# Performance work log

Measured on AMD Instinct MI355X. Metric: run time of the kernel, lower is better.

## Reference

```python
import jax, jax.numpy as jnp
import numpy as np

SCALE_CLS = 7.0
EPS = 1e-12

def _l2norm(x):
    # torch F.normalize: x / max(||x||_2, eps) along last dim
    n = jnp.sqrt(jnp.sum(x * x, axis=-1, keepdims=True))
    return x / jnp.maximum(n, EPS)

def setup_inputs() -> dict:
    key = jax.random.key(0)
    k1, k2 = jax.random.split(key)
    B, Q, C, D, H, W = 4, 75, 5, 512, 6, 6
    ftrain = jax.random.normal(k1, (B, Q, C, D, H, W), dtype=jnp.float32)
    ftest = jax.random.normal(k2, (B, Q, C, D, H, W), dtype=jnp.float32)
    return {"ftrain": ftrain, "ftest": ftest, "K": 28}

def reference(ftrain, ftest, K):
    B, Q, C, D, H, W = ftrain.shape
    P = H * W  # 36 spatial positions
    # spatial means -> [B,Q,C,1,D]
    ftest_mean = ftest.mean(axis=(4, 5))[:, :, :, None, :]
    ftrain_mean = ftrain.mean(axis=(4, 5))[:, :, :, None, :]
    # flatten spatial, move channel last -> [B,Q,C,P,D]
    ft = jnp.swapaxes(ftest.reshape(B, Q, C, D, P), 3, 4)
    fr = jnp.swapaxes(ftrain.reshape(B, Q, C, D, P), 3, 4)
    ft = _l2norm(ft)
    fr = _l2norm(fr)
    ftest_mean = _l2norm(ftest_mean)
    ftrain_mean = _l2norm(ftrain_mean)
    # global scores [B,Q,C]
    scores = SCALE_CLS * jnp.sum(jnp.squeeze(ftest_mean * ftrain_mean), axis=-1)
    # per-position scores [B,Q,C,P]
    ftrain_scores = SCALE_CLS * jnp.sum(ftest_mean * fr, axis=-1)
    ftest_scores = SCALE_CLS * jnp.sum(ft * ftrain_mean, axis=-1)
    # top-K positions (indices distinct, so one-hot-sum mask == gather)
    _, train_ind = jax.lax.top_k(ftrain_scores, K)  # [B,Q,C,K]
    _, test_ind = jax.lax.top_k(ftest_scores, K)
    # gather top-K spatial features and average -> [B,Q,C,D]
    ftest_fuse = jnp.take_along_axis(ft, test_ind[..., None], axis=3).sum(axis=3) / K
    ftrain_fuse = jnp.take_along_axis(fr, train_ind[..., None], axis=3).sum(axis=3) / K
    ftest_fuse = _l2norm(ftest_fuse)
    ftrain_fuse = _l2norm(ftrain_fuse)
    scores_final = SCALE_CLS * jnp.sum(ftest_fuse * ftrain_fuse, axis=-1)
    return (scores, scores_final)
```

## Files before the change

kernel.cpp:

```cpp
#include <hip/hip_runtime.h>
#include <stdint.h>

#define NGRP 1500
#define DD 512
#define PP 36
#define DP (DD*PP)
#define SWEEPS 19
#define SCALE_CLS 7.0f
#define EPS 1e-12f

__device__ __forceinline__ float waveRed(float x){
  #pragma unroll
  for (int off = 32; off; off >>= 1) x += __shfl_xor(x, off, 64);
  return x;
}

__global__ __launch_bounds__(256, 2)
void topk_fuse(const float* __restrict__ gtrain,
               const float* __restrict__ gtest,
               const int* __restrict__ Kp,
               float* __restrict__ out)
{
  __shared__ float s_rt[DD*9];
  __shared__ float s_rr[DD*9];
  __shared__ float s_tm[DD], s_rm[DD];
  __shared__ float s_q[PP], s_e[PP];
  __shared__ float s_a[PP], s_b[PP];
  __shared__ float s_st[PP], s_sr[PP];
  __shared__ float s_nt[PP], s_nr[PP];
  __shared__ float s_wt[PP], s_wr[PP];
  __shared__ float s_red[12];

  const int t    = threadIdx.x;
  const int lane = t & 63;
  const int wave = t >> 6;
  const int g    = blockIdx.x;
  const int K    = Kp[0];
  const int c    = t % 9;
  const int r    = t / 9;
  const bool act = t < 252;

  const float4* gt4 = (const float4*)(gtest  + (size_t)g * DP);
  const float4* gr4 = (const float4*)(gtrain + (size_t)g * DP);

  if (t < PP) { s_q[t] = 0.f; s_e[t] = 0.f; s_a[t] = 0.f; s_b[t] = 0.f; }

  float4 keepT[SWEEPS], keepR[SWEEPS];
  float4 q4 = {0,0,0,0}, e4 = {0,0,0,0};
  #pragma unroll
  for (int k = 0; k < SWEEPS; ++k) {
    const bool cact = (k < SWEEPS-1) ? act : (t < 72);
    float4 T = {0,0,0,0}, R = {0,0,0,0};
    if (cact) { int i = t + 252*k; T = gt4[i]; R = gr4[i]; }
    keepT[k] = T; keepR[k] = R;
    q4.x += T.x*T.x; q4.y += T.y*T.y; q4.z += T.z*T.z; q4.w += T.w*T.w;
    e4.x += R.x*R.x; e4.y += R.y*R.y; e4.z += R.z*R.z; e4.w += R.w*R.w;
    if (cact) {
      s_rt[t + 252*k] = T.x + T.y + T.z + T.w;
      s_rr[t + 252*k] = R.x + R.y + R.z + R.w;
    }
  }
  __syncthreads();

  float pm2 = 0.f, pr2 = 0.f, pmr = 0.f;
  #pragma unroll
  for (int h = 0; h < 2; ++h) {
    int d = t + 256*h;
    float st = 0.f, sr = 0.f;
    #pragma unroll
    for (int j = 0; j < 9; ++j) { st += s_rt[d*9 + j]; sr += s_rr[d*9 + j]; }
    float tm = st * (1.0f/36.0f), rm = sr * (1.0f/36.0f);
    s_tm[d] = tm; s_rm[d] = rm;
    pm2 += tm*tm; pr2 += rm*rm; pmr += tm*rm;
  }
  pm2 = waveRed(pm2); pr2 = waveRed(pr2); pmr = waveRed(pmr);
  if (lane == 0) { s_red[wave] = pm2; s_red[4+wave] = pr2; s_red[8+wave] = pmr; }
  __syncthreads();
  if (t == 0) {
    float m2 = s_red[0]+s_red[1]+s_red[2]+s_red[3];
    float r2 = s_red[4]+s_red[5]+s_red[6]+s_red[7];
    float mr = s_red[8]+s_red[9]+s_red[10]+s_red[11];
    float n1 = fmaxf(sqrtf(m2), EPS), n2 = fmaxf(sqrtf(r2), EPS);
    out[g] = SCALE_CLS * mr / (n1 * n2);
  }

  float4 a4 = {0,0,0,0}, b4 = {0,0,0,0};
  #pragma unroll
  for (int k = 0; k < SWEEPS; ++k) {
    int d = r + 28*k; if (d > 511) d = 511;
    float tm = s_tm[d], rm = s_rm[d];
    float4 T = keepT[k], R = keepR[k];
    a4.x += T.x*rm; a4.y += T.y*rm; a4.z += T.z*rm; a4.w += T.w*rm;
    b4.x += R.x*tm; b4.y += R.y*tm; b4.z += R.z*tm; b4.w += R.w*tm;
  }
  if (act) {
    int p0 = c*4;
    atomicAdd(&s_q[p0+0], q4.x); atomicAdd(&s_q[p0+1], q4.y);
    atomicAdd(&s_q[p0+2], q4.z); atomicAdd(&s_q[p0+3], q4.w);
    atomicAdd(&s_e[p0+0], e4.x); atomicAdd(&s_e[p0+1], e4.y);
    atomicAdd(&s_e[p0+2], e4.z); atomicAdd(&s_e[p0+3], e4.w);
    atomicAdd(&s_a[p0+0], a4.x); atomicAdd(&s_a[p0+1], a4.y);
    atomicAdd(&s_a[p0+2], a4.z); atomicAdd(&s_a[p0+3], a4.w);
    atomicAdd(&s_b[p0+0], b4.x); atomicAdd(&s_b[p0+1], b4.y);
    atomicAdd(&s_b[p0+2], b4.z); atomicAdd(&s_b[p0+3], b4.w);
  }
  __syncthreads();

  if (wave < 2 && lane < PP) {
    float q  = wave ? s_e[lane] : s_q[lane];
    float dm = wave ? s_b[lane] : s_a[lane];
    float n  = fmaxf(sqrtf(q), EPS);
    if (wave) { s_nr[lane] = n; s_sr[lane] = dm / n; }
    else      { s_nt[lane] = n; s_st[lane] = dm / n; }
  }
  __syncthreads();

  if (wave < 2 && lane < PP) {
    const float* sc = wave ? s_sr : s_st;
    const float* nn = wave ? s_nr : s_nt;
    float*       w  = wave ? s_wr : s_wt;
    float mine = sc[lane];
    int rank = 0;
    #pragma unroll
    for (int p = 0; p < PP; ++p) {
      float o = sc[p];
      rank += ((o > mine) || (o == mine && p < lane)) ? 1 : 0;
    }
    w[lane] = (rank < K) ? (1.0f / nn[lane]) : 0.f;
  }
  __syncthreads();

  float wt0=0,wt1=0,wt2=0,wt3=0, wr0=0,wr1=0,wr2=0,wr3=0;
  if (act) {
    wt0 = s_wt[4*c+0]; wt1 = s_wt[4*c+1]; wt2 = s_wt[4*c+2]; wt3 = s_wt[4*c+3];
    wr0 = s_wr[4*c+0]; wr1 = s_wr[4*c+1]; wr2 = s_wr[4*c+2]; wr3 = s_wr[4*c+3];
  }
  #pragma unroll
  for (int k = 0; k < SWEEPS; ++k) {
    const bool cact = (k < SWEEPS-1) ? act : (t < 72);
    if (cact) {
      float4 T = keepT[k], R = keepR[k];
      s_rt[t + 252*k] = T.x*wt0 + T.y*wt1 + T.z*wt2 + T.w*wt3;
      s_rr[t + 252*k] = R.x*wr0 + R.y*wr1 + R.z*wr2 + R.w*wr3;
    }
  }
  __syncthreads();
  float U2 = 0.f, V2 = 0.f, UV = 0.f;
  #pragma unroll
  for (int h = 0; h < 2; ++h) {
    int d = t + 256*h;
    float u = 0.f, v = 0.f;
    #pragma unroll
    for (int j = 0; j < 9; ++j) { u += s_rt[d*9 + j]; v += s_rr[d*9 + j]; }
    U2 += u*u; V2 += v*v; UV += u*v;
  }
  U2 = waveRed(U2); V2 = waveRed(V2); UV = waveRed(UV);
  if (lane == 0) { s_red[wave] = U2; s_red[4+wave] = V2; s_red[8+wave] = UV; }
  __syncthreads();
  if (t == 0) {
    float u2 = s_red[0]+s_red[1]+s_red[2]+s_red[3];
    float v2 = s_red[4]+s_red[5]+s_red[6]+s_red[7];
    float uv = s_red[8]+s_red[9]+s_red[10]+s_red[11];
    float nu = fmaxf(sqrtf(u2), EPS), nv = fmaxf(sqrtf(v2), EPS);
    out[NGRP + g] = SCALE_CLS * uv / (nu * nv);
  }
}

extern "C" void kernel_launch(void* const* d_in, const int* in_sizes, int n_in,
                              void* d_out, int out_size, void* d_ws, size_t ws_size,
                              hipStream_t stream)
{
  const float* ftrain = (const float*)d_in[0];
  const float* ftest  = (const float*)d_in[1];
  const int*   Kp     = (const int*)d_in[2];
  float*       out    = (float*)d_out;
  topk_fuse<<<NGRP, 256, 0, stream>>>(ftrain, ftest, Kp, out);
}
```

Baseline: 268.9 us.

## Stage full tiles in LDS via direct global-to-LDS loads with 512 threads

Replaces the register-held float4 sweeps with asynchronous global_load_lds transfers that copy each group's full test and train tiles (144 KB of LDS) into shared memory. The block grows to 512 threads with one channel per thread. Partial waitcnt overlaps the test-tile reductions with the train-tile load. Per-position reductions now run as strided LDS loops, and the top-K fuse becomes a weighted dot against the shared weights, which removes the second staging pass. The large LDS footprint limits occupancy to about one block per CU and leaves little latency hiding across blocks.

```diff
diff --git a/kernel.cpp b/kernel.cpp
--- a/kernel.cpp
+++ b/kernel.cpp
@@ -2,10 +2,9 @@
 #include <stdint.h>
 
 #define NGRP 1500
-#define DD 512
-#define PP 36
-#define DP (DD*PP)
-#define SWEEPS 19
+#define DD   512
+#define PP   36
+#define DP   (DD*PP)
 #define SCALE_CLS 7.0f
 #define EPS 1e-12f
 
@@ -15,103 +14,135 @@
   return x;
 }
 
-__global__ __launch_bounds__(256, 2)
+__global__ __launch_bounds__(512)
 void topk_fuse(const float* __restrict__ gtrain,
                const float* __restrict__ gtest,
                const int* __restrict__ Kp,
                float* __restrict__ out)
 {
-  __shared__ float s_rt[DD*9];
-  __shared__ float s_rr[DD*9];
+  __shared__ float sT[DP];
+  __shared__ float sR[DP];
   __shared__ float s_tm[DD], s_rm[DD];
-  __shared__ float s_q[PP], s_e[PP];
-  __shared__ float s_a[PP], s_b[PP];
+  __shared__ __align__(16) float s_q[PP];
+  __shared__ __align__(16) float s_e[PP];
+  __shared__ __align__(16) float s_a[PP];
+  __shared__ __align__(16) float s_b[PP];
+  __shared__ __align__(16) float s_wt[PP];
+  __shared__ __align__(16) float s_wr[PP];
+  __shared__ float s_nt[PP], s_nr[PP];
   __shared__ float s_st[PP], s_sr[PP];
-  __shared__ float s_nt[PP], s_nr[PP];
-  __shared__ float s_wt[PP], s_wr[PP];
-  __shared__ float s_red[12];
+  __shared__ float s_red[24];
 
   const int t    = threadIdx.x;
   const int lane = t & 63;
   const int wave = t >> 6;
   const int g    = blockIdx.x;
   const int K    = Kp[0];
-  const int c    = t % 9;
-  const int r    = t / 9;
-  const bool act = t < 252;
-
-  const float4* gt4 = (const float4*)(gtest  + (size_t)g * DP);
-  const float4* gr4 = (const float4*)(gtrain + (size_t)g * DP);
+
+  const char* gT = (const char*)(gtest  + (size_t)g * DP);
+  const char* gR = (const char*)(gtrain + (size_t)g * DP);
+  char* sTc = (char*)sT;
+  char* sRc = (char*)sR;
 
   if (t < PP) { s_q[t] = 0.f; s_e[t] = 0.f; s_a[t] = 0.f; s_b[t] = 0.f; }
 
-  float4 keepT[SWEEPS], keepR[SWEEPS];
-  float4 q4 = {0,0,0,0}, e4 = {0,0,0,0};
-  #pragma unroll
-  for (int k = 0; k < SWEEPS; ++k) {
-    const bool cact = (k < SWEEPS-1) ? act : (t < 72);
-    float4 T = {0,0,0,0}, R = {0,0,0,0};
-    if (cact) { int i = t + 252*k; T = gt4[i]; R = gr4[i]; }
-    keepT[k] = T; keepR[k] = R;
-    q4.x += T.x*T.x; q4.y += T.y*T.y; q4.z += T.z*T.z; q4.w += T.w*T.w;
-    e4.x += R.x*R.x; e4.y += R.y*R.y; e4.z += R.z*R.z; e4.w += R.w*R.w;
-    if (cact) {
-      s_rt[t + 252*k] = T.x + T.y + T.z + T.w;
-      s_rr[t + 252*k] = R.x + R.y + R.z + R.w;
-    }
-  }
-  __syncthreads();
-
-  float pm2 = 0.f, pr2 = 0.f, pmr = 0.f;
-  #pragma unroll
-  for (int h = 0; h < 2; ++h) {
-    int d = t + 256*h;
-    float st = 0.f, sr = 0.f;
-    #pragma unroll
-    for (int j = 0; j < 9; ++j) { st += s_rt[d*9 + j]; sr += s_rr[d*9 + j]; }
-    float tm = st * (1.0f/36.0f), rm = sr * (1.0f/36.0f);
-    s_tm[d] = tm; s_rm[d] = rm;
-    pm2 += tm*tm; pr2 += rm*rm; pmr += tm*rm;
-  }
-  pm2 = waveRed(pm2); pr2 = waveRed(pr2); pmr = waveRed(pmr);
-  if (lane == 0) { s_red[wave] = pm2; s_red[4+wave] = pr2; s_red[8+wave] = pmr; }
-  __syncthreads();
+  {
+    const int base = wave * 9216;
+    #pragma unroll
+    for (int s = 0; s < 9; ++s) {
+      const int off = base + s * 1024;
+      __builtin_amdgcn_global_load_lds((const uint32_t*)(gT + off + lane*16),
+                                       (uint32_t*)(sTc + off), 16, 0, 0);
+    }
+    #pragma unroll
+    for (int s = 0; s < 9; ++s) {
+      const int off = base + s * 1024;
+      __builtin_amdgcn_global_load_lds((const uint32_t*)(gR + off + lane*16),
+                                       (uint32_t*)(sRc + off), 16, 0, 0);
+    }
+  }
+
+  asm volatile("s_waitcnt vmcnt(9) lgkmcnt(0)" ::: "memory");
+  __builtin_amdgcn_s_barrier();
+  __builtin_amdgcn_sched_barrier(0);
+
+  float tm;
+  {
+    const float4* r4 = (const float4*)(sT + t * PP);
+    float s = 0.f;
+    #pragma unroll
+    for (int j = 0; j < 9; ++j) {
+      float4 x = r4[j];
+      s += (x.x + x.y) + (x.z + x.w);
+    }
+    tm = s * (1.0f / 36.0f);
+    s_tm[t] = tm;
+  }
+  {
+    float pm2 = waveRed(tm * tm);
+    if (lane == 0) s_red[wave] = pm2;
+  }
+
+  if (t < 504) {
+    const int p = t % 36, c = t / 36;
+    float q = 0.f;
+    for (int d = c; d < DD; d += 14) { float x = sT[d*PP + p]; q += x * x; }
+    atomicAdd(&s_q[p], q);
+  }
+
+  asm volatile("s_waitcnt vmcnt(0) lgkmcnt(0)" ::: "memory");
+  __builtin_amdgcn_s_barrier();
+  __builtin_amdgcn_sched_barrier(0);
+
+  float rm;
+  {
+    const float4* r4 = (const float4*)(sR + t * PP);
+    float s = 0.f;
+    #pragma unroll
+    for (int j = 0; j < 9; ++j) {
+      float4 x = r4[j];
+      s += (x.x + x.y) + (x.z + x.w);
+    }
+    rm = s * (1.0f / 36.0f);
+    s_rm[t] = rm;
+  }
+  {
+    float pr2 = waveRed(rm * rm);
+    float pmr = waveRed(rm * tm);
+    if (lane == 0) { s_red[8 + wave] = pr2; s_red[16 + wave] = pmr; }
+  }
+  __syncthreads();
+
   if (t == 0) {
-    float m2 = s_red[0]+s_red[1]+s_red[2]+s_red[3];
-    float r2 = s_red[4]+s_red[5]+s_red[6]+s_red[7];
-    float mr = s_red[8]+s_red[9]+s_red[10]+s_red[11];
-    float n1 = fmaxf(sqrtf(m2), EPS), n2 = fmaxf(sqrtf(r2), EPS);
-    out[g] = SCALE_CLS * mr / (n1 * n2);
-  }
-
-  float4 a4 = {0,0,0,0}, b4 = {0,0,0,0};
-  #pragma unroll
-  for (int k = 0; k < SWEEPS; ++k) {
-    int d = r + 28*k; if (d > 511) d = 511;
-    float tm = s_tm[d], rm = s_rm[d];
-    float4 T = keepT[k], R = keepR[k];
-    a4.x += T.x*rm; a4.y += T.y*rm; a4.z += T.z*rm; a4.w += T.w*rm;
-    b4.x += R.x*tm; b4.y += R.y*tm; b4.z += R.z*tm; b4.w += R.w*tm;
-  }
-  if (act) {
-    int p0 = c*4;
-    atomicAdd(&s_q[p0+0], q4.x); atomicAdd(&s_q[p0+1], q4.y);
-    atomicAdd(&s_q[p0+2], q4.z); atomicAdd(&s_q[p0+3], q4.w);
-    atomicAdd(&s_e[p0+0], e4.x); atomicAdd(&s_e[p0+1], e4.y);
-    atomicAdd(&s_e[p0+2], e4.z); atomicAdd(&s_e[p0+3], e4.w);
-    atomicAdd(&s_a[p0+0], a4.x); atomicAdd(&s_a[p0+1], a4.y);
-    atomicAdd(&s_a[p0+2], a4.z); atomicAdd(&s_a[p0+3], a4.w);
-    atomicAdd(&s_b[p0+0], b4.x); atomicAdd(&s_b[p0+1], b4.y);
-    atomicAdd(&s_b[p0+2], b4.z); atomicAdd(&s_b[p0+3], b4.w);
+    float m2 = 0.f, r2 = 0.f, mr = 0.f;
+    #pragma unroll
+    for (int w = 0; w < 8; ++w) {
+      m2 += s_red[w]; r2 += s_red[8 + w]; mr += s_red[16 + w];
+    }
+    out[g] = SCALE_CLS * mr / (fmaxf(sqrtf(m2), EPS) * fmaxf(sqrtf(r2), EPS));
+  }
+
+  if (t < 504) {
+    const int p = t % 36, c = t / 36;
+    float a = 0.f, e = 0.f, b = 0.f;
+    for (int d = c; d < DD; d += 14) {
+      const int i = d * PP + p;
+      float x = sT[i], y = sR[i];
+      a += x * s_rm[d];
+      e += y * y;
+      b += y * s_tm[d];
+    }
+    atomicAdd(&s_a[p], a); atomicAdd(&s_e[p], e); atomicAdd(&s_b[p], b);
   }
   __syncthreads();
 
   if (wave < 2 && lane < PP) {
-    float q  = wave ? s_e[lane] : s_q[lane];
-    float dm = wave ? s_b[lane] : s_a[lane];
-    float n  = fmaxf(sqrtf(q), EPS);
-    if (wave) { s_nr[lane] = n; s_sr[lane] = dm / n; }
-    else      { s_nt[lane] = n; s_st[lane] = dm / n; }
+    const float* qq = wave ? s_e : s_q;
+    const float* dm = wave ? s_b : s_a;
+    float n  = fmaxf(sqrtf(qq[lane]), EPS);
+    float sc = dm[lane] / n;
+    if (wave) { s_nr[lane] = n; s_sr[lane] = sc; }
+    else      { s_nt[lane] = n; s_st[lane] = sc; }
   }
   __syncthreads();
 
@@ -130,39 +161,31 @@
   }
   __syncthreads();
 
-  float wt0=0,wt1=0,wt2=0,wt3=0, wr0=0,wr1=0,wr2=0,wr3=0;
-  if (act) {
-    wt0 = s_wt[4*c+0]; wt1 = s_wt[4*c+1]; wt2 = s_wt[4*c+2]; wt3 = s_wt[4*c+3];
-    wr0 = s_wr[4*c+0]; wr1 = s_wr[4*c+1]; wr2 = s_wr[4*c+2]; wr3 = s_wr[4*c+3];
-  }
-  #pragma unroll
-  for (int k = 0; k < SWEEPS; ++k) {
-    const bool cact = (k < SWEEPS-1) ? act : (t < 72);
-    if (cact) {
-      float4 T = keepT[k], R = keepR[k];
-      s_rt[t + 252*k] = T.x*wt0 + T.y*wt1 + T.z*wt2 + T.w*wt3;
-      s_rr[t + 252*k] = R.x*wr0 + R.y*wr1 + R.z*wr2 + R.w*wr3;
-    }
-  }
-  __syncthreads();
-  float U2 = 0.f, V2 = 0.f, UV = 0.f;
-  #pragma unroll
-  for (int h = 0; h < 2; ++h) {
-    int d = t + 256*h;
-    float u = 0.f, v = 0.f;
-    #pragma unroll
-    for (int j = 0; j < 9; ++j) { u += s_rt[d*9 + j]; v += s_rr[d*9 + j]; }
-    U2 += u*u; V2 += v*v; UV += u*v;
-  }
-  U2 = waveRed(U2); V2 = waveRed(V2); UV = waveRed(UV);
-  if (lane == 0) { s_red[wave] = U2; s_red[4+wave] = V2; s_red[8+wave] = UV; }
+  {
+    const float4* rt = (const float4*)(sT + t * PP);
+    const float4* rr = (const float4*)(sR + t * PP);
+    const float4* w4t = (const float4*)s_wt;
+    const float4* w4r = (const float4*)s_wr;
+    float U = 0.f, V = 0.f;
+    #pragma unroll
+    for (int j = 0; j < 9; ++j) {
+      float4 x = rt[j], y = rr[j], a4 = w4t[j], b4 = w4r[j];
+      U += x.x*a4.x + x.y*a4.y + x.z*a4.z + x.w*a4.w;
+      V += y.x*b4.x + y.y*b4.y + y.z*b4.z + y.w*b4.w;
+    }
+    float u2 = waveRed(U * U);
+    float v2 = waveRed(V * V);
+    float uv = waveRed(U * V);
+    if (lane == 0) { s_red[wave] = u2; s_red[8 + wave] = v2; s_red[16 + wave] = uv; }
+  }
   __syncthreads();
   if (t == 0) {
-    float u2 = s_red[0]+s_red[1]+s_red[2]+s_red[3];
-    float v2 = s_red[4]+s_red[5]+s_red[6]+s_red[7];
-    float uv = s_red[8]+s_red[9]+s_red[10]+s_red[11];
-    float nu = fmaxf(sqrtf(u2), EPS), nv = fmaxf(sqrtf(v2), EPS);
-    out[NGRP + g] = SCALE_CLS * uv / (nu * nv);
+    float u2 = 0.f, v2 = 0.f, uv = 0.f;
+    #pragma unroll
+    for (int w = 0; w < 8; ++w) {
+      u2 += s_red[w]; v2 += s_red[8 + w]; uv += s_red[16 + w];
+    }
+    out[NGRP + g] = SCALE_CLS * uv / (fmaxf(sqrtf(u2), EPS) * fmaxf(sqrtf(v2), EPS));
   }
 }
 
@@ -174,5 +197,5 @@
   const float* ftest  = (const float*)d_in[1];
   const int*   Kp     = (const int*)d_in[2];
   float*       out    = (float*)d_out;
-  topk_fuse<<<NGRP, 256, 0, stream>>>(ftrain, ftest, Kp, out);
+  topk_fuse<<<NGRP, 512, 0, stream>>>(ftrain, ftest, Kp, out);
 }
```

After: 271.3 us. Within noise of the previous version (+0.9%).
